# Kernel optimization log

Measured on AMD Instinct MI355X. Metric: run time of the kernel, lower is better.

## Reference

```python
import jax, jax.numpy as jnp
import numpy as np
import math

B, T, P, E, H = 4, 64, 256, 512, 8
D = E // H
LN_EPS = 1e-5


def setup_inputs() -> dict:
    key = jax.random.key(0)
    ks = jax.random.split(key, 6)
    s = 0.02  # weight init scale
    return {
        "x": jax.random.normal(ks[0], (B, T, P, E), jnp.float32),
        "Wq": jax.random.normal(ks[1], (E, E), jnp.float32) * s,
        "bq": jnp.zeros((E,), jnp.float32),
        "Wk": jax.random.normal(ks[2], (E, E), jnp.float32) * s,
        "bk": jnp.zeros((E,), jnp.float32),
        "Wv": jax.random.normal(ks[3], (E, E), jnp.float32) * s,
        "bv": jnp.zeros((E,), jnp.float32),
        "Wo": jax.random.normal(ks[4], (E, E), jnp.float32) * s,
        "bo": jnp.zeros((E,), jnp.float32),
        "ln_g": jnp.ones((E,), jnp.float32),
        "ln_b": jnp.zeros((E,), jnp.float32),
    }


def _proj(x, W, b):
    # torch nn.Linear: y = x @ W.T + b
    return jnp.einsum('btpe,fe->btpf', x, W) + b


def _heads(y):
    # b t p (h d) -> b p h t d
    b, t, p, e = y.shape
    return y.reshape(b, t, p, H, D).transpose(0, 2, 3, 1, 4)


def reference(x, Wq, bq, Wk, bk, Wv, bv, Wo, bo, ln_g, ln_b):
    b, t, p, e = x.shape
    q = _heads(_proj(x, Wq, bq))  # [B,P,H,T,D]
    k = _heads(_proj(x, Wk, bk))
    v = _heads(_proj(x, Wv, bv))

    scores = jnp.einsum('bphtd,bphsd->bphts', q, k) / math.sqrt(D)
    causal_mask = jnp.triu(jnp.ones((t, t), dtype=bool), k=1)  # True above diag
    scores = jnp.where(causal_mask, -jnp.inf, scores)
    attn = jax.nn.softmax(scores, axis=-1)
    o = jnp.einsum('bphts,bphsd->bphtd', attn, v)

    # b p h t d -> b t p (h d)
    o = o.transpose(0, 3, 1, 2, 4).reshape(b, t, p, e)
    attn_out = jnp.einsum('btpe,fe->btpf', o, Wo) + bo

    y = x + attn_out
    # AdaptiveNormalizer with conditioning=None -> plain LayerNorm over E
    mu = jnp.mean(y, axis=-1, keepdims=True)
    var = jnp.var(y, axis=-1, keepdims=True)
    return (y - mu) * jax.lax.rsqrt(var + LN_EPS) * ln_g + ln_b
```

## Files before the change

kernel.cpp:

```cpp
#include <hip/hip_runtime.h>
#include <stdint.h>

#define B_ 4
#define T_ 64
#define P_ 256
#define E_ 512
#define H_ 8
#define D_ 64
#define NF 1536
#define MCH 16384

typedef unsigned short u16;
typedef __attribute__((ext_vector_type(8))) __bf16 bf16x8;
typedef __attribute__((ext_vector_type(4))) float f32x4;
typedef __attribute__((ext_vector_type(16))) float f32x16;

__device__ __forceinline__ u16 f2bf(float x) {
  union { float f; uint32_t u; } a; a.f = x;
  uint32_t u = a.u;
  uint32_t r = (u + 0x7FFFu + ((u >> 16) & 1u)) >> 16;
  return (u16)r;
}

__device__ __forceinline__ bf16x8 ld8(const u16* p) {
  union { uint4 u; bf16x8 b; } t;
  t.u = *reinterpret_cast<const uint4*>(p);
  return t.b;
}

typedef __attribute__((address_space(3))) void lds_void;
typedef __attribute__((address_space(1))) void g_void;
__device__ __forceinline__ void gl_lds16(const void* g, void* l) {
  __builtin_amdgcn_global_load_lds((g_void*)g, (lds_void*)l, 16, 0, 0);
}

__device__ __forceinline__ f32x4 mfma16(bf16x8 a, bf16x8 b, f32x4 c) {
  return __builtin_amdgcn_mfma_f32_16x16x32_bf16(a, b, c, 0, 0, 0);
}
__device__ __forceinline__ f32x16 mfma32(bf16x8 a, bf16x8 b, f32x16 c) {
  return __builtin_amdgcn_mfma_f32_32x32x16_bf16(a, b, c, 0, 0, 0);
}

#define SBAR() __builtin_amdgcn_s_barrier()

__global__ void cvt_bf16(const float* __restrict__ src, u16* __restrict__ dst, int n8) {
  int i = blockIdx.x * blockDim.x + threadIdx.x;
  if (i >= n8) return;
  const float4* s = reinterpret_cast<const float4*>(src) + (size_t)i * 2;
  float4 a = s[0], b = s[1];
  union { u16 u[8]; uint4 v; } t;
  t.u[0] = f2bf(a.x); t.u[1] = f2bf(a.y); t.u[2] = f2bf(a.z); t.u[3] = f2bf(a.w);
  t.u[4] = f2bf(b.x); t.u[5] = f2bf(b.y); t.u[6] = f2bf(b.z); t.u[7] = f2bf(b.w);
  reinterpret_cast<uint4*>(dst)[i] = t.v;
}

__global__ void cvt_w(const float* __restrict__ Wq, const float* __restrict__ Wk,
                      const float* __restrict__ Wv, const float* __restrict__ Wo,
                      u16* __restrict__ wqkv, u16* __restrict__ wobf) {
  int idx = blockIdx.x * blockDim.x + threadIdx.x;
  int w = idx >> 15;
  int off = idx & 32767;
  const float* s = (w == 0) ? Wq : (w == 1) ? Wk : (w == 2) ? Wv : Wo;
  const float4* sp = reinterpret_cast<const float4*>(s) + (size_t)off * 2;
  float4 a = sp[0], b = sp[1];
  union { u16 u[8]; uint4 v; } t;
  t.u[0] = f2bf(a.x); t.u[1] = f2bf(a.y); t.u[2] = f2bf(a.z); t.u[3] = f2bf(a.w);
  t.u[4] = f2bf(b.x); t.u[5] = f2bf(b.y); t.u[6] = f2bf(b.z); t.u[7] = f2bf(b.w);
  if (w < 3) reinterpret_cast<uint4*>(wqkv)[w * 32768 + off] = t.v;
  else       reinterpret_cast<uint4*>(wobf)[off] = t.v;
}

#define GQ_READA(E, HH, MB)                                                 \
  _Pragma("unroll") for (int i = 0; i < 2; i++)                             \
  _Pragma("unroll") for (int q = 0; q < 2; q++)                             \
    af[i][q] = ld8(ldsA + ((E) * 2 + (HH)) * 8192 +                         \
                   (wr * 128 + ((MB) + i) * 32 + l31) * 32 +                \
                   ((q * 2 + lhi) ^ xkey) * 8);

#define GQ_READB(E, HH)                                                     \
  _Pragma("unroll") for (int j = 0; j < 2; j++)                             \
  _Pragma("unroll") for (int q = 0; q < 2; q++)                             \
    bfv[j][q] = ld8(ldsB + ((E) * 2 + (HH)) * 8192 +                        \
                    (wc * 64 + j * 32 + l31) * 32 +                         \
                    ((q * 2 + lhi) ^ xkey) * 8);

#define GQ_MFMA(MB)                                                         \
  __builtin_amdgcn_s_setprio(1);                                            \
  _Pragma("unroll") for (int i = 0; i < 2; i++)                             \
  _Pragma("unroll") for (int j = 0; j < 2; j++)                             \
  _Pragma("unroll") for (int q = 0; q < 2; q++)                             \
    acc[(MB) + i][j] = mfma32(af[i][q], bfv[j][q], acc[(MB) + i][j]);       \
  __builtin_amdgcn_s_setprio(0);

#define GQ_KLOOP()                                                          \
  stageA(0, 0, 0); stageB(0, 0, 0);                                         \
  stageA(0, 1, 0); stageB(0, 1, 0);                                         \
  stageA(1, 0, 1); stageB(1, 0, 1);                                         \
  asm volatile("s_waitcnt vmcnt(8)" ::: "memory");                          \
  SBAR();                                                                   \
  _Pragma("unroll 2") for (int s = 0; s < 8; ++s) {                         \
    const int e = s & 1;                                                    \
    bf16x8 af[2][2], bfv[2][2];                                             \
    GQ_READA(e, 0, 0)                                                       \
    GQ_READB(e, 0)                                                          \
    if (s < 7) stageA(e ^ 1, 1, s + 1);                                     \
    SBAR();                                                                 \
    GQ_MFMA(0)                                                              \
    SBAR();                                                                 \
    GQ_READA(e, 0, 2)                                                       \
    if (s < 7) stageB(e ^ 1, 1, s + 1);                                     \
    if (s < 7) { asm volatile("s_waitcnt vmcnt(8)" ::: "memory"); }         \
    else       { asm volatile("s_waitcnt vmcnt(0)" ::: "memory"); }         \
    SBAR();                                                                 \
    GQ_MFMA(2)                                                              \
    SBAR();                                                                 \
    GQ_READA(e, 1, 0)                                                       \
    GQ_READB(e, 1)                                                          \
    if (s < 6) stageA(e, 0, s + 2);                                         \
    SBAR();                                                                 \
    GQ_MFMA(0)                                                              \
    SBAR();                                                                 \
    GQ_READA(e, 1, 2)                                                       \
    if (s < 6) stageB(e, 0, s + 2);                                         \
    if (s < 6)      { asm volatile("s_waitcnt vmcnt(8)" ::: "memory"); }    \
    else if (s == 6){ asm volatile("s_waitcnt vmcnt(4)" ::: "memory"); }    \
    SBAR();                                                                 \
    GQ_MFMA(2)                                                              \
    SBAR();                                                                 \
  }

__global__ __launch_bounds__(512, 2) void k1_qkv(
    const u16* __restrict__ xbf,
    const u16* __restrict__ wqkv,
    const float* __restrict__ bq, const float* __restrict__ bk, const float* __restrict__ bv,
    u16* __restrict__ qkv)
{
  __shared__ u16 lds[65536];
  u16* ldsA = lds;
  u16* ldsB = lds + 32768;

  const int tid = threadIdx.x;
  const int lane = tid & 63, wid = tid >> 6;
  const int wr = wid >> 2, wc = wid & 3;
  const int l31 = lane & 31, lhi = lane >> 5;
  const int xkey = (l31 >> 1) & 3;

  const int cpx = gridDim.x >> 3;
  const int logical = (blockIdx.x & 7) * cpx + (blockIdx.x >> 3);
  const int m0 = (logical / 6) * 256;
  const int n0 = (logical % 6) * 256;

  const u16* ga = xbf + (size_t)m0 * E_;
  const u16* gb = wqkv + (size_t)n0 * E_;

  const int r0 = tid >> 2;
  const int c0 = ((tid & 3) ^ ((tid >> 3) & 3)) * 8;

  auto stageA = [&](int e, int h, int kt) {
    const int kc = kt * 64 + h * 32;
    u16* base = ldsA + (e * 2 + h) * 8192;
    gl_lds16(ga + (size_t)r0 * E_ + kc + c0, base + wid * 512);
    gl_lds16(ga + (size_t)(r0 + 128) * E_ + kc + c0, base + 4096 + wid * 512);
  };
  auto stageB = [&](int e, int h, int kt) {
    const int kc = kt * 64 + h * 32;
    u16* base = ldsB + (e * 2 + h) * 8192;
    gl_lds16(gb + (size_t)r0 * E_ + kc + c0, base + wid * 512);
    gl_lds16(gb + (size_t)(r0 + 128) * E_ + kc + c0, base + 4096 + wid * 512);
  };

  f32x16 acc[4][2];
#pragma unroll
  for (int i = 0; i < 4; i++)
#pragma unroll
    for (int j = 0; j < 2; j++)
#pragma unroll
      for (int r = 0; r < 16; r++) acc[i][j][r] = 0.f;

  GQ_KLOOP()

  float bias2[2];
#pragma unroll
  for (int j = 0; j < 2; j++) {
    const int fcol = n0 + wc * 64 + j * 32 + l31;
    bias2[j] = fcol < 512 ? bq[fcol] : (fcol < 1024 ? bk[fcol - 512] : bv[fcol - 1024]);
  }
  const int fbase = n0 + wc * 64 + l31;
#pragma unroll
  for (int mi = 0; mi < 4; mi++)
#pragma unroll
    for (int r = 0; r < 16; r++) {
      const size_t row = m0 + wr * 128 + mi * 32 + (r & 3) + 8 * (r >> 2) + 4 * lhi;
      u16* dst = qkv + row * NF + fbase;
      dst[0]  = f2bf(acc[mi][0][r] + bias2[0]);
      dst[32] = f2bf(acc[mi][1][r] + bias2[1]);
    }
}

__global__ __launch_bounds__(256) void k2_attn(
    const u16* __restrict__ qkv,
    u16* __restrict__ o)
{
  __shared__ u16 Pl[4][64 * 72];
  const int tid = threadIdx.x, lane = tid & 63, wid = tid >> 6;
  const int gw = blockIdx.x * 4 + wid;
  const int b = gw >> 11;
  const int g = gw & 2047;
  const int h = g & 7, p = g >> 3;
  const int g4 = lane >> 4;
  const size_t ts = (size_t)P_ * NF;
  const u16* qb = qkv + (size_t)b * MCH * NF + (size_t)p * NF + h * D_;
  const u16* kb = qb + 512;
  const u16* vb = qb + 1024;
  u16* ob = o + (size_t)b * MCH * E_;

  bf16x8 qf[4][2], kf[4][2];
#pragma unroll
  for (int i = 0; i < 4; i++)
#pragma unroll
    for (int ks = 0; ks < 2; ks++) {
      const int rr = i * 16 + (lane & 15);
      const int dc = ks * 32 + g4 * 8;
      qf[i][ks] = ld8(qb + (size_t)rr * ts + dc);
      kf[i][ks] = ld8(kb + (size_t)rr * ts + dc);
    }

  bf16x8 vfr[2][4];
#pragma unroll
  for (int ks = 0; ks < 2; ks++)
#pragma unroll
    for (int ni = 0; ni < 4; ni++) {
      union { u16 u[8]; bf16x8 b; } tv;
#pragma unroll
      for (int j = 0; j < 8; j++) {
        const int s = ks * 32 + g4 * 8 + j;
        tv.u[j] = vb[(size_t)s * ts + ni * 16 + (lane & 15)];
      }
      vfr[ks][ni] = tv.b;
    }

  f32x4 S[4][4];
#pragma unroll
  for (int i = 0; i < 4; i++)
#pragma unroll
    for (int j = 0; j < 4; j++) { f32x4 z = {0.f, 0.f, 0.f, 0.f}; S[i][j] = z; }
#pragma unroll
  for (int ks = 0; ks < 2; ks++)
#pragma unroll
    for (int mi = 0; mi < 4; mi++)
#pragma unroll
      for (int ni = 0; ni < 4; ni++)
        if (ni <= mi)
          S[mi][ni] = mfma16(qf[mi][ks], kf[ni][ks], S[mi][ni]);

  u16* pw = &Pl[wid][0];
#pragma unroll
  for (int mi = 0; mi < 4; mi++)
#pragma unroll
    for (int r = 0; r < 4; r++) {
      const int t = mi * 16 + g4 * 4 + r;
      float v[4]; float mx = -1e30f;
#pragma unroll
      for (int ni = 0; ni < 4; ni++) {
        const int s = ni * 16 + (lane & 15);
        v[ni] = (s <= t) ? S[mi][ni][r] * 0.125f : -1e30f;
        mx = fmaxf(mx, v[ni]);
      }
      mx = fmaxf(mx, __shfl_xor(mx, 1));
      mx = fmaxf(mx, __shfl_xor(mx, 2));
      mx = fmaxf(mx, __shfl_xor(mx, 4));
      mx = fmaxf(mx, __shfl_xor(mx, 8));
      float sum = 0.f; float pv[4];
#pragma unroll
      for (int ni = 0; ni < 4; ni++) {
        const int s = ni * 16 + (lane & 15);
        pv[ni] = (s <= t) ? __expf(v[ni] - mx) : 0.f;
        sum += pv[ni];
      }
      sum += __shfl_xor(sum, 1);
      sum += __shfl_xor(sum, 2);
      sum += __shfl_xor(sum, 4);
      sum += __shfl_xor(sum, 8);
      const float inv = 1.0f / sum;
#pragma unroll
      for (int ni = 0; ni < 4; ni++) {
        const int s = ni * 16 + (lane & 15);
        pw[t * 72 + s] = f2bf(pv[ni] * inv);
      }
    }
  asm volatile("s_waitcnt lgkmcnt(0)" ::: "memory");

  f32x4 O[4][4];
#pragma unroll
  for (int i = 0; i < 4; i++)
#pragma unroll
    for (int j = 0; j < 4; j++) { f32x4 z = {0.f, 0.f, 0.f, 0.f}; O[i][j] = z; }
#pragma unroll
  for (int ks = 0; ks < 2; ks++) {
    bf16x8 pa[4];
#pragma unroll
    for (int mi = 0; mi < 4; mi++)
      pa[mi] = ld8(pw + (mi * 16 + (lane & 15)) * 72 + ks * 32 + g4 * 8);
#pragma unroll
    for (int mi = 0; mi < 4; mi++)
#pragma unroll
      for (int ni = 0; ni < 4; ni++)
        if (!(ks == 1 && mi < 2))
          O[mi][ni] = mfma16(pa[mi], vfr[ks][ni], O[mi][ni]);
  }
#pragma unroll
  for (int mi = 0; mi < 4; mi++)
#pragma unroll
    for (int ni = 0; ni < 4; ni++)
#pragma unroll
      for (int r = 0; r < 4; r++) {
        const int t = mi * 16 + g4 * 4 + r;
        const int d = ni * 16 + (lane & 15);
        ob[((size_t)t * P_ + p) * E_ + h * D_ + d] = f2bf(O[mi][ni][r]);
      }
}

__global__ __launch_bounds__(512, 2) void k3_gemm(
    const u16* __restrict__ obf,
    const u16* __restrict__ wo,
    const float* __restrict__ bo,
    const float* __restrict__ x,
    u16* __restrict__ yb)
{
  __shared__ u16 lds[65536];
  u16* ldsA = lds;
  u16* ldsB = lds + 32768;

  const int tid = threadIdx.x;
  const int lane = tid & 63, wid = tid >> 6;
  const int wr = wid >> 2, wc = wid & 3;
  const int l31 = lane & 31, lhi = lane >> 5;
  const int xkey = (l31 >> 1) & 3;

  const int cpx = gridDim.x >> 3;
  const int logical = (blockIdx.x & 7) * cpx + (blockIdx.x >> 3);
  const int m0 = (logical >> 1) * 256;
  const int n0 = (logical & 1) * 256;

  const u16* ga = obf + (size_t)m0 * E_;
  const u16* gb = wo + (size_t)n0 * E_;

  const int r0 = tid >> 2;
  const int c0 = ((tid & 3) ^ ((tid >> 3) & 3)) * 8;

  auto stageA = [&](int e, int h, int kt) {
    const int kc = kt * 64 + h * 32;
    u16* base = ldsA + (e * 2 + h) * 8192;
    gl_lds16(ga + (size_t)r0 * E_ + kc + c0, base + wid * 512);
    gl_lds16(ga + (size_t)(r0 + 128) * E_ + kc + c0, base + 4096 + wid * 512);
  };
  auto stageB = [&](int e, int h, int kt) {
    const int kc = kt * 64 + h * 32;
    u16* base = ldsB + (e * 2 + h) * 8192;
    gl_lds16(gb + (size_t)r0 * E_ + kc + c0, base + wid * 512);
    gl_lds16(gb + (size_t)(r0 + 128) * E_ + kc + c0, base + 4096 + wid * 512);
  };

  f32x16 acc[4][2];
#pragma unroll
  for (int i = 0; i < 4; i++)
#pragma unroll
    for (int j = 0; j < 2; j++)
#pragma unroll
      for (int r = 0; r < 16; r++) acc[i][j][r] = 0.f;

  GQ_KLOOP()

  float bias2[2];
#pragma unroll
  for (int j = 0; j < 2; j++)
    bias2[j] = bo[n0 + wc * 64 + j * 32 + l31];
  const int fbase = n0 + wc * 64 + l31;
#pragma unroll
  for (int mi = 0; mi < 4; mi++)
#pragma unroll
    for (int r = 0; r < 16; r++) {
      const size_t row = m0 + wr * 128 + mi * 32 + (r & 3) + 8 * (r >> 2) + 4 * lhi;
      u16* dst = yb + row * E_ + fbase;
      const float* xr = x + row * E_ + fbase;
      dst[0]  = f2bf(acc[mi][0][r] + bias2[0] + xr[0]);
      dst[32] = f2bf(acc[mi][1][r] + bias2[1] + xr[32]);
    }
}

__global__ __launch_bounds__(256) void k3_ln(
    const u16* __restrict__ yb, const float* __restrict__ lng,
    const float* __restrict__ lnb, float* __restrict__ out)
{
  const int lane = threadIdx.x & 63;
  const size_t row = (size_t)blockIdx.x * 4 + (threadIdx.x >> 6);
  const int c = lane * 8;
  const uint4 d = *reinterpret_cast<const uint4*>(yb + row * E_ + c);
  const uint32_t* dw = reinterpret_cast<const uint32_t*>(&d);
  float f[8];
#pragma unroll
  for (int j = 0; j < 4; j++) {
    union { uint32_t u; float v; } lo, hi;
    lo.u = dw[j] << 16; hi.u = dw[j] & 0xffff0000u;
    f[2 * j] = lo.v; f[2 * j + 1] = hi.v;
  }
  float s = 0.f, q = 0.f;
#pragma unroll
  for (int j = 0; j < 8; j++) { s += f[j]; q += f[j] * f[j]; }
#pragma unroll
  for (int d2 = 1; d2 < 64; d2 <<= 1) { s += __shfl_xor(s, d2); q += __shfl_xor(q, d2); }
  const float mean = s * (1.0f / 512.0f);
  const float var = q * (1.0f / 512.0f) - mean * mean;
  const float rs = rsqrtf(var + 1e-5f);
  float o8[8];
#pragma unroll
  for (int j = 0; j < 8; j++)
    o8[j] = (f[j] - mean) * rs * lng[c + j] + lnb[c + j];
  float4* op = reinterpret_cast<float4*>(out + row * E_ + c);
  op[0] = make_float4(o8[0], o8[1], o8[2], o8[3]);
  op[1] = make_float4(o8[4], o8[5], o8[6], o8[7]);
}

extern "C" void kernel_launch(void* const* d_in, const int* in_sizes, int n_in,
                              void* d_out, int out_size, void* d_ws, size_t ws_size,
                              hipStream_t stream) {
  const float* x   = (const float*)d_in[0];
  const float* Wq  = (const float*)d_in[1];
  const float* bq  = (const float*)d_in[2];
  const float* Wk  = (const float*)d_in[3];
  const float* bk  = (const float*)d_in[4];
  const float* Wv  = (const float*)d_in[5];
  const float* bv  = (const float*)d_in[6];
  const float* Wo  = (const float*)d_in[7];
  const float* bo  = (const float*)d_in[8];
  const float* lng = (const float*)d_in[9];
  const float* lnb = (const float*)d_in[10];
  float* out = (float*)d_out;
  uint8_t* ws = (uint8_t*)d_ws;

  const size_t NEED_BIG = 270532608ULL;
  if (ws_size >= NEED_BIG) {
    u16* wqkv = (u16*)(ws);
    u16* wobf = (u16*)(ws + 1572864);
    u16* xbf  = (u16*)(ws + 2097152);
    u16* qkvc = (u16*)(ws + 69206016);
    u16* obf  = xbf;
    u16* yb   = qkvc;

    cvt_w<<<512, 256, 0, stream>>>(Wq, Wk, Wv, Wo, wqkv, wobf);
    cvt_bf16<<<16384, 256, 0, stream>>>(x, xbf, B_ * MCH * E_ / 8);
    k1_qkv<<<1536, 512, 0, stream>>>(xbf, wqkv, bq, bk, bv, qkvc);
    k2_attn<<<2048, 256, 0, stream>>>(qkvc, obf);
    k3_gemm<<<512, 512, 0, stream>>>(obf, wobf, bo, x, yb);
    k3_ln<<<16384, 256, 0, stream>>>(yb, lng, lnb, out);
  } else {
    u16* xbf  = (u16*)(ws);
    u16* qkvc = (u16*)(ws + 16777216);
    u16* obf  = (u16*)(ws + 67108864);
    u16* wqkv = (u16*)(ws + 83886080);
    u16* wobf = (u16*)(ws + 85458944);
    u16* yb   = qkvc;

    cvt_w<<<512, 256, 0, stream>>>(Wq, Wk, Wv, Wo, wqkv, wobf);
    for (int b = 0; b < B_; ++b) {
      const float* xb = x + (size_t)b * MCH * E_;
      cvt_bf16<<<4096, 256, 0, stream>>>(xb, xbf, MCH * E_ / 8);
      k1_qkv<<<384, 512, 0, stream>>>(xbf, wqkv, bq, bk, bv, qkvc);
      k2_attn<<<512, 256, 0, stream>>>(qkvc, obf);
      k3_gemm<<<128, 512, 0, stream>>>(obf, wobf, bo, xb, yb);
      k3_ln<<<4096, 256, 0, stream>>>(yb, lng, lnb, out + (size_t)b * MCH * E_);
    }
  }
}
```

Measured before the change: 361.0 us.

## Fuse conversion kernels and coarsen QKV GEMM k-loop to fewer barriers

The x and weight fp32-to-bf16 conversions are merged into one launch, removing a kernel launch and its tail. The QKV GEMM inner loop now reads all four A fragments at once and runs 16 MFMAs per phase, where it previously ran two 8-MFMA halves. This halves the number of barriers and groups the A and B global-to-LDS stages together. The cost is more live A-fragment registers, which could hurt occupancy at launch_bounds(512,2), and less interleaving of loads with compute.

Result: no change. 360.0 us, median of 3 (-0.3%).

```diff
diff --git a/kernel.cpp b/kernel.cpp
--- a/kernel.cpp
+++ b/kernel.cpp
@@ -42,6 +42,32 @@
 }
 
 #define SBAR() __builtin_amdgcn_s_barrier()
+
+__global__ void cvt_all(const float* __restrict__ x,
+                        const float* __restrict__ Wq, const float* __restrict__ Wk,
+                        const float* __restrict__ Wv, const float* __restrict__ Wo,
+                        u16* __restrict__ xbf, u16* __restrict__ wqkv,
+                        u16* __restrict__ wobf) {
+  const int idx = blockIdx.x * blockDim.x + threadIdx.x;
+  const float* s;
+  uint4* d;
+  if (idx < 4194304) {
+    s = x + (size_t)idx * 8;
+    d = reinterpret_cast<uint4*>(xbf) + idx;
+  } else {
+    const int k = idx - 4194304;
+    const int w = k >> 15, off = k & 32767;
+    s = ((w == 0) ? Wq : (w == 1) ? Wk : (w == 2) ? Wv : Wo) + (size_t)off * 8;
+    d = (w < 3) ? reinterpret_cast<uint4*>(wqkv) + w * 32768 + off
+                : reinterpret_cast<uint4*>(wobf) + off;
+  }
+  const float4* sp = reinterpret_cast<const float4*>(s);
+  float4 a = sp[0], b = sp[1];
+  union { u16 u[8]; uint4 v; } t;
+  t.u[0] = f2bf(a.x); t.u[1] = f2bf(a.y); t.u[2] = f2bf(a.z); t.u[3] = f2bf(a.w);
+  t.u[4] = f2bf(b.x); t.u[5] = f2bf(b.y); t.u[6] = f2bf(b.z); t.u[7] = f2bf(b.w);
+  *d = t.v;
+}
 
 __global__ void cvt_bf16(const float* __restrict__ src, u16* __restrict__ dst, int n8) {
   int i = blockIdx.x * blockDim.x + threadIdx.x;
@@ -53,7 +79,6 @@
   t.u[4] = f2bf(b.x); t.u[5] = f2bf(b.y); t.u[6] = f2bf(b.z); t.u[7] = f2bf(b.w);
   reinterpret_cast<uint4*>(dst)[i] = t.v;
 }
-
 __global__ void cvt_w(const float* __restrict__ Wq, const float* __restrict__ Wk,
                       const float* __restrict__ Wv, const float* __restrict__ Wo,
                       u16* __restrict__ wqkv, u16* __restrict__ wobf) {
@@ -70,11 +95,11 @@
   else       reinterpret_cast<uint4*>(wobf)[off] = t.v;
 }
 
-#define GQ_READA(E, HH, MB)                                                 \
-  _Pragma("unroll") for (int i = 0; i < 2; i++)                             \
+#define GQ_READA4(E, HH)                                                    \
+  _Pragma("unroll") for (int i = 0; i < 4; i++)                             \
   _Pragma("unroll") for (int q = 0; q < 2; q++)                             \
     af[i][q] = ld8(ldsA + ((E) * 2 + (HH)) * 8192 +                         \
-                   (wr * 128 + ((MB) + i) * 32 + l31) * 32 +                \
+                   (wr * 128 + i * 32 + l31) * 32 +                         \
                    ((q * 2 + lhi) ^ xkey) * 8);
 
 #define GQ_READB(E, HH)                                                     \
@@ -84,12 +109,12 @@
                     (wc * 64 + j * 32 + l31) * 32 +                         \
                     ((q * 2 + lhi) ^ xkey) * 8);
 
-#define GQ_MFMA(MB)                                                         \
+#define GQ_MFMA16()                                                         \
   __builtin_amdgcn_s_setprio(1);                                            \
-  _Pragma("unroll") for (int i = 0; i < 2; i++)                             \
+  _Pragma("unroll") for (int i = 0; i < 4; i++)                             \
   _Pragma("unroll") for (int j = 0; j < 2; j++)                             \
   _Pragma("unroll") for (int q = 0; q < 2; q++)                             \
-    acc[(MB) + i][j] = mfma32(af[i][q], bfv[j][q], acc[(MB) + i][j]);       \
+    acc[i][j] = mfma32(af[i][q], bfv[j][q], acc[i][j]);                     \
   __builtin_amdgcn_s_setprio(0);
 
 #define GQ_KLOOP()                                                          \
@@ -100,32 +125,24 @@
   SBAR();                                                                   \
   _Pragma("unroll 2") for (int s = 0; s < 8; ++s) {                         \
     const int e = s & 1;                                                    \
-    bf16x8 af[2][2], bfv[2][2];                                             \
-    GQ_READA(e, 0, 0)                                                       \
+    bf16x8 af[4][2], bfv[2][2];                                             \
+                                                   \
+    GQ_READA4(e, 0)                                                         \
     GQ_READB(e, 0)                                                          \
-    if (s < 7) stageA(e ^ 1, 1, s + 1);                                     \
-    SBAR();                                                                 \
-    GQ_MFMA(0)                                                              \
-    SBAR();                                                                 \
-    GQ_READA(e, 0, 2)                                                       \
-    if (s < 7) stageB(e ^ 1, 1, s + 1);                                     \
-    if (s < 7) { asm volatile("s_waitcnt vmcnt(8)" ::: "memory"); }         \
+    if (s < 7) { stageA(e ^ 1, 1, s + 1); stageB(e ^ 1, 1, s + 1);          \
+                 asm volatile("s_waitcnt vmcnt(8)" ::: "memory"); }         \
     else       { asm volatile("s_waitcnt vmcnt(0)" ::: "memory"); }         \
     SBAR();                                                                 \
-    GQ_MFMA(2)                                                              \
+    GQ_MFMA16()                                                             \
     SBAR();                                                                 \
-    GQ_READA(e, 1, 0)                                                       \
+                                                   \
+    GQ_READA4(e, 1)                                                         \
     GQ_READB(e, 1)                                                          \
-    if (s < 6) stageA(e, 0, s + 2);                                         \
-    SBAR();                                                                 \
-    GQ_MFMA(0)                                                              \
-    SBAR();                                                                 \
-    GQ_READA(e, 1, 2)                                                       \
-    if (s < 6) stageB(e, 0, s + 2);                                         \
-    if (s < 6)      { asm volatile("s_waitcnt vmcnt(8)" ::: "memory"); }    \
+    if (s < 6)      { stageA(e, 0, s + 2); stageB(e, 0, s + 2);             \
+                      asm volatile("s_waitcnt vmcnt(8)" ::: "memory"); }    \
     else if (s == 6){ asm volatile("s_waitcnt vmcnt(4)" ::: "memory"); }    \
     SBAR();                                                                 \
-    GQ_MFMA(2)                                                              \
+    GQ_MFMA16()                                                             \
     SBAR();                                                                 \
   }
 
@@ -447,8 +464,7 @@
     u16* obf  = xbf;
     u16* yb   = qkvc;
 
-    cvt_w<<<512, 256, 0, stream>>>(Wq, Wk, Wv, Wo, wqkv, wobf);
-    cvt_bf16<<<16384, 256, 0, stream>>>(x, xbf, B_ * MCH * E_ / 8);
+    cvt_all<<<16896, 256, 0, stream>>>(x, Wq, Wk, Wv, Wo, xbf, wqkv, wobf);
     k1_qkv<<<1536, 512, 0, stream>>>(xbf, wqkv, bq, bk, bv, qkvc);
     k2_attn<<<2048, 256, 0, stream>>>(qkvc, obf);
     k3_gemm<<<512, 512, 0, stream>>>(obf, wobf, bo, x, yb);
```
